# Kernel optimization log

Measured on AMD Instinct MI355X. Metric: run time of the kernel, lower is better.

The kernel has to match this reference:

```python
import jax, jax.numpy as jnp
import numpy as np


def setup_inputs() -> dict:
    key = jax.random.key(0)
    ks = jax.random.split(key, 7)
    B, T, E, H = 4, 4096, 1024, 64
    return {
        "idx": jax.random.normal(ks[0], (B, T, E), dtype=jnp.float32),
        "Wq": jax.random.normal(ks[1], (E, H), dtype=jnp.float32) * (E ** -0.5),
        "bq": jax.random.normal(ks[2], (H,), dtype=jnp.float32) * 0.01,
        "Wk": jax.random.normal(ks[3], (E, H), dtype=jnp.float32) * (E ** -0.5),
        "bk": jax.random.normal(ks[4], (H,), dtype=jnp.float32) * 0.01,
        "Wv": jax.random.normal(ks[5], (E, H), dtype=jnp.float32) * (E ** -0.5),
        "bv": jax.random.normal(ks[6], (H,), dtype=jnp.float32) * 0.01,
    }


def reference(idx, Wq, bq, Wk, bk, Wv, bv):
    # idx: [B, T, E]
    d = idx.shape[-1]  # note: torch code scales by n_embd**-0.5, NOT head_size
    Q = idx @ Wq + bq  # [B, T, H]
    K = idx @ Wk + bk
    V = idx @ Wv + bv
    # scores; NOTE: original torch code calls wei.masked_fill(...) non-in-place
    # and discards the result, so no causal mask is applied. No softmax either.
    wei = jnp.einsum("bth,bsh->bts", Q, K) * (d ** -0.5)  # [B, T, T]
    out = jnp.einsum("bts,bsh->bth", wei, V)  # [B, T, H]
    return out
```

## Files before the change

kernel.cpp:

```cpp
#include <hip/hip_runtime.h>


typedef __attribute__((ext_vector_type(8))) short bf16x8;
typedef __attribute__((ext_vector_type(4))) float f32x4;

#define MFMA16(a, b, c) __builtin_amdgcn_mfma_f32_16x16x32_bf16((a), (b), (c), 0, 0, 0)

__device__ __forceinline__ unsigned short f2bf(float f) {
    unsigned int u = __float_as_uint(f);
    u += 0x7fffu + ((u >> 16) & 1u);
    return (unsigned short)(u >> 16);
}

__global__ void prep(const float* __restrict__ Wq, const float* __restrict__ Wk,
                     const float* __restrict__ Wv, unsigned short* __restrict__ WB,
                     float* __restrict__ Mf) {
    int t = blockIdx.x * 256 + threadIdx.x;
    if (t < 16384) Mf[t] = 0.f;
    int kki = t / 768;
    int rem = t - kki * 768;
    int nt = rem >> 6, lane = rem & 63;
    int n = nt * 16 + (lane & 15);
    int kb = kki * 32 + ((lane >> 4) * 8);
    int mm = n >> 6, h = n & 63;
    const float* W = (mm == 0) ? Wq : (mm == 1) ? Wk : Wv;
    float sc = (mm == 1) ? 0.03125f : 1.0f;
    bf16x8 v;
    #pragma unroll
    for (int j = 0; j < 8; j++) v[j] = (short)f2bf(W[(size_t)(kb + j) * 64 + h] * sc);
    *(bf16x8*)(WB + (size_t)t * 8) = v;
}

__global__ __launch_bounds__(256, 2) void qkv(
    const float* __restrict__ idx, const unsigned short* __restrict__ WB,
    const float* __restrict__ bq, const float* __restrict__ bk, const float* __restrict__ bv,
    unsigned short* __restrict__ Q, unsigned short* __restrict__ Kt,
    unsigned short* __restrict__ Vt) {
    __shared__ unsigned short As[32 * 1032];
    const int lane = threadIdx.x & 63, w = threadIdx.x >> 6;
    const int r0 = blockIdx.x * 32;

    const float* src = idx + (size_t)(r0 + w * 8) * 1024;
    #pragma unroll
    for (int batch = 0; batch < 4; batch++) {
        float4 v[8];
        #pragma unroll
        for (int j = 0; j < 8; j++)
            v[j] = *(const float4*)(src + (size_t)(batch * 8 + j) * 256 + lane * 4);
        #pragma unroll
        for (int j = 0; j < 8; j++) {
            int i   = batch * 8 + j;
            int row = w * 8 + (i >> 2);
            int k   = (i & 3) * 256 + lane * 4;
            unsigned int lo = ((unsigned int)f2bf(v[j].y) << 16) | f2bf(v[j].x);
            unsigned int hi = ((unsigned int)f2bf(v[j].w) << 16) | f2bf(v[j].z);
            uint2 p; p.x = lo; p.y = hi;
            *(uint2*)(As + (size_t)row * 1032 + k) = p;
        }
    }
    __syncthreads();

    const f32x4 z4 = {0.f, 0.f, 0.f, 0.f};
    f32x4 acc[2][3] = {{z4, z4, z4}, {z4, z4, z4}};

    const unsigned short* a_base0 = As + (size_t)(lane & 15) * 1032 + ((lane >> 4) * 8);
    const unsigned short* a_base1 = a_base0 + 16 * 1032;
    bf16x8 a_c[2], b0[3], b1[3], b2[3];
    a_c[0] = *(const bf16x8*)a_base0;
    a_c[1] = *(const bf16x8*)a_base1;
    {
        const unsigned short* Bp0 = WB + (size_t)(lane * 8);
        const unsigned short* Bp1 = WB + (size_t)(12 * 64 + lane) * 8;
        #pragma unroll
        for (int j = 0; j < 3; j++) {
            b0[j] = *(const bf16x8*)(Bp0 + (w + j * 4) * 512);
            b1[j] = *(const bf16x8*)(Bp1 + (w + j * 4) * 512);
            b2[j] = b1[j];
        }
    }
    for (int kk = 0; kk < 32; kk++) {
        bf16x8 na0 = a_c[0], na1 = a_c[1];
        if (kk < 30) {
            const unsigned short* Bp = WB + (size_t)(((kk + 2) * 12) * 64 + lane) * 8;
            #pragma unroll
            for (int j = 0; j < 3; j++) b2[j] = *(const bf16x8*)(Bp + (w + j * 4) * 512);
        }
        if (kk < 31) {
            na0 = *(const bf16x8*)(a_base0 + (kk + 1) * 32);
            na1 = *(const bf16x8*)(a_base1 + (kk + 1) * 32);
        }
        #pragma unroll
        for (int j = 0; j < 3; j++) {
            acc[0][j] = MFMA16(a_c[0], b0[j], acc[0][j]);
            acc[1][j] = MFMA16(a_c[1], b0[j], acc[1][j]);
        }
        #pragma unroll
        for (int j = 0; j < 3; j++) { b0[j] = b1[j]; b1[j] = b2[j]; }
        a_c[0] = na0; a_c[1] = na1;
    }

    __syncthreads();
    unsigned short* Lq = As;
    unsigned short* Lk = As + 2048;
    unsigned short* Lv = As + 4096;
    const int h     = w * 16 + (lane & 15);
    const int rbase = (lane >> 4) * 4;
    {
        float bias0 = bq[h], bias1 = bk[h] * 0.03125f, bias2 = bv[h];
        #pragma unroll
        for (int rf = 0; rf < 2; rf++) {
            #pragma unroll
            for (int reg = 0; reg < 4; reg++) {
                int r = rf * 16 + rbase + reg;
                Lq[r * 64 + h] = f2bf(acc[rf][0][reg] + bias0);
                Lk[h * 32 + r] = f2bf(acc[rf][1][reg] + bias1);
                Lv[h * 32 + r] = f2bf(acc[rf][2][reg] + bias2);
            }
        }
    }
    __syncthreads();
    {
        const int tt = threadIdx.x;
        int qr = tt >> 3, qh = (tt & 7) * 8;
        *(uint4*)(Q + (size_t)(r0 + qr) * 64 + qh) = *(const uint4*)(Lq + qr * 64 + qh);
        int b = r0 >> 12, t0 = r0 & 4095;
        int hh = tt >> 2, tc = (tt & 3) * 8;
        *(uint4*)(Kt + (size_t)b * 262144 + hh * 4096 + t0 + tc) =
            *(const uint4*)(Lk + hh * 32 + tc);
        *(uint4*)(Vt + (size_t)b * 262144 + hh * 4096 + t0 + tc) =
            *(const uint4*)(Lv + hh * 32 + tc);
    }
}

__global__ __launch_bounds__(256) void ktv(
    const unsigned short* __restrict__ Kt, const unsigned short* __restrict__ Vt,
    float* __restrict__ Mf) {
    const int lane = threadIdx.x & 63, wave = threadIdx.x >> 6;
    const int c = blockIdx.x, b = blockIdx.y;
    const unsigned short* Kb = Kt + (size_t)b * 262144;
    const unsigned short* Vb = Vt + (size_t)b * 262144;
    const f32x4 z4 = {0.f, 0.f, 0.f, 0.f};
    f32x4 acc[4] = {z4, z4, z4, z4};
    const int m  = 16 * wave + (lane & 15);
    const int tq = (lane >> 4) * 8;
    #pragma unroll
    for (int it = 0; it < 4; it++) {
        int t0 = c * 128 + it * 32 + tq;
        bf16x8 a = *(const bf16x8*)&Kb[(size_t)m * 4096 + t0];
        #pragma unroll
        for (int nt = 0; nt < 4; nt++) {
            bf16x8 bb = *(const bf16x8*)&Vb[(size_t)(nt * 16 + (lane & 15)) * 4096 + t0];
            acc[nt] = MFMA16(a, bb, acc[nt]);
        }
    }
    float* P = Mf + (size_t)b * 4096;
    const int rowb = 16 * wave + (lane >> 4) * 4;
    #pragma unroll
    for (int nt = 0; nt < 4; nt++)
        #pragma unroll
        for (int reg = 0; reg < 4; reg++)
            atomicAdd(&P[(rowb + reg) * 64 + nt * 16 + (lane & 15)], acc[nt][reg]);
}

__global__ __launch_bounds__(256) void qm(
    const unsigned short* __restrict__ Q, const float* __restrict__ Mf,
    float* __restrict__ out) {
    __shared__ unsigned short Lm[64 * 72];
    const int lane = threadIdx.x & 63, wave = threadIdx.x >> 6;
    const int r0 = blockIdx.x * 64;
    const int b  = r0 >> 12;
    {
        const int tt = threadIdx.x;
        int h1 = tt >> 2, h2c = (tt & 3) * 16;
        const float* Mp = Mf + (size_t)b * 4096 + h1 * 64 + h2c;
        float vals[16];
        *(float4*)(vals + 0)  = *(const float4*)(Mp + 0);
        *(float4*)(vals + 4)  = *(const float4*)(Mp + 4);
        *(float4*)(vals + 8)  = *(const float4*)(Mp + 8);
        *(float4*)(vals + 12) = *(const float4*)(Mp + 12);
        #pragma unroll
        for (int u = 0; u < 16; u++) Lm[(h2c + u) * 72 + h1] = f2bf(vals[u]);
    }
    __syncthreads();
    const f32x4 z4 = {0.f, 0.f, 0.f, 0.f};
    f32x4 acc[4] = {z4, z4, z4, z4};
    const int rr = r0 + 16 * wave + (lane & 15);
    const int kq = (lane >> 4) * 8;
    #pragma unroll
    for (int ks = 0; ks < 2; ks++) {
        int k0 = ks * 32;
        bf16x8 a = *(const bf16x8*)&Q[(size_t)rr * 64 + k0 + kq];
        #pragma unroll
        for (int nt = 0; nt < 4; nt++) {
            bf16x8 bb = *(const bf16x8*)&Lm[(size_t)(nt * 16 + (lane & 15)) * 72 + k0 + kq];
            acc[nt] = MFMA16(a, bb, acc[nt]);
        }
    }
    const int rowb = r0 + 16 * wave + (lane >> 4) * 4;
    #pragma unroll
    for (int nt = 0; nt < 4; nt++)
        #pragma unroll
        for (int reg = 0; reg < 4; reg++)
            out[(size_t)(rowb + reg) * 64 + nt * 16 + (lane & 15)] = acc[nt][reg];
}

extern "C" void kernel_launch(void* const* d_in, const int* in_sizes, int n_in,
                              void* d_out, int out_size, void* d_ws, size_t ws_size,
                              hipStream_t stream) {
    const float* idx = (const float*)d_in[0];
    const float* Wq  = (const float*)d_in[1];
    const float* bq  = (const float*)d_in[2];
    const float* Wk  = (const float*)d_in[3];
    const float* bk  = (const float*)d_in[4];
    const float* Wv  = (const float*)d_in[5];
    const float* bv  = (const float*)d_in[6];
    float* out = (float*)d_out;

    char* ws = (char*)d_ws;
    unsigned short* WB = (unsigned short*)(ws);
    float*          Mf = (float*)(ws + (1024u << 10));
    unsigned short* Q  = (unsigned short*)(ws + (2048u << 10));
    unsigned short* Kt = (unsigned short*)(ws + (4096u << 10));
    unsigned short* Vt = (unsigned short*)(ws + (6144u << 10));

    hipLaunchKernelGGL(prep, dim3(96),    dim3(256), 0, stream, Wq, Wk, Wv, WB, Mf);
    hipLaunchKernelGGL(qkv,  dim3(512),   dim3(256), 0, stream,
                       idx, WB, bq, bk, bv, Q, Kt, Vt);
    hipLaunchKernelGGL(ktv,  dim3(32, 4), dim3(256), 0, stream, Kt, Vt, Mf);
    hipLaunchKernelGGL(qm,   dim3(256),   dim3(256), 0, stream, Q, Mf, out);
}
```

Baseline: 121.9 us.

## Fuse all stages into one cooperative persistent kernel with grid syncs

Replaces the four-kernel pipeline (weight prep, QKV projection, K^T V reduction, Q·M) with a single cooperative kernel that uses grid.sync between phases. Q stays in shared memory across phases, and each block writes a per-block partial K^T V that is then reduced by 64 blocks. This is meant to remove launch gaps and the global round-trip of Q/K/V. The cost is three grid-wide barriers and a larger partial buffer. If the cooperative launch fails, the code falls back to the old kernels.

```diff
diff --git a/kernel.cpp b/kernel.cpp
--- a/kernel.cpp
+++ b/kernel.cpp
@@ -1,4 +1,7 @@
 #include <hip/hip_runtime.h>
+#include <hip/hip_cooperative_groups.h>
+
+namespace cg = cooperative_groups;
 
 
 typedef __attribute__((ext_vector_type(8))) short bf16x8;
@@ -10,6 +13,180 @@
     unsigned int u = __float_as_uint(f);
     u += 0x7fffu + ((u >> 16) & 1u);
     return (unsigned short)(u >> 16);
+}
+
+__global__ __launch_bounds__(256, 2) void mega(
+    const float* __restrict__ idx,
+    const float* __restrict__ Wq, const float* __restrict__ bq_,
+    const float* __restrict__ Wk, const float* __restrict__ bk_,
+    const float* __restrict__ Wv, const float* __restrict__ bv_,
+    unsigned short* __restrict__ WB, float* __restrict__ part,
+    unsigned short* __restrict__ Mt, float* __restrict__ out) {
+    __shared__ unsigned short As[32 * 1032];
+    __shared__ unsigned short Lq[32 * 68];
+    unsigned short* Lk = As;
+    unsigned short* Lv = As + 64 * 36;
+
+    const int tid = threadIdx.x, lane = tid & 63, w = tid >> 6;
+    const int bid = blockIdx.x;
+    cg::grid_group grid = cg::this_grid();
+
+    if (bid < 96) {
+        int t = bid * 256 + tid;
+        int kki = t / 768;
+        int rem = t - kki * 768;
+        int nt = rem >> 6, l = rem & 63;
+        int n = nt * 16 + (l & 15);
+        int kb = kki * 32 + ((l >> 4) * 8);
+        int mm = n >> 6, h = n & 63;
+        const float* W = (mm == 0) ? Wq : (mm == 1) ? Wk : Wv;
+        float sc = (mm == 1) ? 0.03125f : 1.0f;
+        bf16x8 v;
+        #pragma unroll
+        for (int j = 0; j < 8; j++) v[j] = (short)f2bf(W[(size_t)(kb + j) * 64 + h] * sc);
+        *(bf16x8*)(WB + (size_t)t * 8) = v;
+    }
+    grid.sync();
+
+    const int r0 = bid * 32;
+    {
+        const float* src = idx + (size_t)(r0 + w * 8) * 1024;
+        #pragma unroll
+        for (int batch = 0; batch < 4; batch++) {
+            float4 v[8];
+            #pragma unroll
+            for (int j = 0; j < 8; j++)
+                v[j] = *(const float4*)(src + (size_t)(batch * 8 + j) * 256 + lane * 4);
+            #pragma unroll
+            for (int j = 0; j < 8; j++) {
+                int i   = batch * 8 + j;
+                int row = w * 8 + (i >> 2);
+                int k   = (i & 3) * 256 + lane * 4;
+                unsigned int lo = ((unsigned int)f2bf(v[j].y) << 16) | f2bf(v[j].x);
+                unsigned int hi = ((unsigned int)f2bf(v[j].w) << 16) | f2bf(v[j].z);
+                uint2 p; p.x = lo; p.y = hi;
+                *(uint2*)(As + (size_t)row * 1032 + k) = p;
+            }
+        }
+    }
+    __syncthreads();
+
+    const f32x4 z4 = {0.f, 0.f, 0.f, 0.f};
+    f32x4 acc[2][3] = {{z4, z4, z4}, {z4, z4, z4}};
+    {
+        const unsigned short* a_base0 = As + (size_t)(lane & 15) * 1032 + ((lane >> 4) * 8);
+        const unsigned short* a_base1 = a_base0 + 16 * 1032;
+        bf16x8 a_c[2], b0[3], b1[3], b2[3];
+        a_c[0] = *(const bf16x8*)a_base0;
+        a_c[1] = *(const bf16x8*)a_base1;
+        {
+            const unsigned short* Bp0 = WB + (size_t)(lane * 8);
+            const unsigned short* Bp1 = WB + (size_t)(12 * 64 + lane) * 8;
+            #pragma unroll
+            for (int j = 0; j < 3; j++) {
+                b0[j] = *(const bf16x8*)(Bp0 + (w + j * 4) * 512);
+                b1[j] = *(const bf16x8*)(Bp1 + (w + j * 4) * 512);
+                b2[j] = b1[j];
+            }
+        }
+        for (int kk = 0; kk < 32; kk++) {
+            bf16x8 na0 = a_c[0], na1 = a_c[1];
+            if (kk < 30) {
+                const unsigned short* Bp = WB + (size_t)(((kk + 2) * 12) * 64 + lane) * 8;
+                #pragma unroll
+                for (int j = 0; j < 3; j++) b2[j] = *(const bf16x8*)(Bp + (w + j * 4) * 512);
+            }
+            if (kk < 31) {
+                na0 = *(const bf16x8*)(a_base0 + (kk + 1) * 32);
+                na1 = *(const bf16x8*)(a_base1 + (kk + 1) * 32);
+            }
+            #pragma unroll
+            for (int j = 0; j < 3; j++) {
+                acc[0][j] = MFMA16(a_c[0], b0[j], acc[0][j]);
+                acc[1][j] = MFMA16(a_c[1], b0[j], acc[1][j]);
+            }
+            #pragma unroll
+            for (int j = 0; j < 3; j++) { b0[j] = b1[j]; b1[j] = b2[j]; }
+            a_c[0] = na0; a_c[1] = na1;
+        }
+    }
+
+    __syncthreads();
+    {
+        const int h     = w * 16 + (lane & 15);
+        const int rbase = (lane >> 4) * 4;
+        float bias0 = bq_[h], bias1 = bk_[h] * 0.03125f, bias2 = bv_[h];
+        #pragma unroll
+        for (int rf = 0; rf < 2; rf++) {
+            #pragma unroll
+            for (int reg = 0; reg < 4; reg++) {
+                int r = rf * 16 + rbase + reg;
+                Lq[r * 68 + h] = f2bf(acc[rf][0][reg] + bias0);
+                Lk[h * 36 + r] = f2bf(acc[rf][1][reg] + bias1);
+                Lv[h * 36 + r] = f2bf(acc[rf][2][reg] + bias2);
+            }
+        }
+    }
+    __syncthreads();
+
+    {
+        const int tq = (lane >> 4) * 8;
+        bf16x8 a = *(const bf16x8*)&Lk[(16 * w + (lane & 15)) * 36 + tq];
+        f32x4 accM[4];
+        #pragma unroll
+        for (int nt = 0; nt < 4; nt++) {
+            bf16x8 bb = *(const bf16x8*)&Lv[(nt * 16 + (lane & 15)) * 36 + tq];
+            accM[nt] = MFMA16(a, bb, z4);
+        }
+        float* P = part + (size_t)bid * 4096;
+        const int rowb = 16 * w + (lane >> 4) * 4;
+        #pragma unroll
+        for (int nt = 0; nt < 4; nt++)
+            #pragma unroll
+            for (int reg = 0; reg < 4; reg++)
+                P[(rowb + reg) * 64 + nt * 16 + (lane & 15)] = accM[nt][reg];
+    }
+    grid.sync();
+
+    if (bid < 64) {
+        int i = bid * 256 + tid;
+        int b = i >> 12, e = i & 4095;
+        const float* Pp = part + (size_t)(b * 128) * 4096 + e;
+        float s0 = 0.f, s1 = 0.f, s2 = 0.f, s3 = 0.f;
+        #pragma unroll 4
+        for (int j = 0; j < 128; j += 4) {
+            s0 += Pp[(size_t)(j + 0) * 4096];
+            s1 += Pp[(size_t)(j + 1) * 4096];
+            s2 += Pp[(size_t)(j + 2) * 4096];
+            s3 += Pp[(size_t)(j + 3) * 4096];
+        }
+        Mt[(size_t)b * 4096 + (e & 63) * 64 + (e >> 6)] = f2bf((s0 + s1) + (s2 + s3));
+    }
+    grid.sync();
+
+    {
+        const int rf = w >> 1, np = w & 1;
+        const int b  = r0 >> 12;
+        const int kq = (lane >> 4) * 8;
+        f32x4 acc4[2] = {z4, z4};
+        #pragma unroll
+        for (int ks = 0; ks < 2; ks++) {
+            bf16x8 a = *(const bf16x8*)&Lq[(rf * 16 + (lane & 15)) * 68 + ks * 32 + kq];
+            #pragma unroll
+            for (int j = 0; j < 2; j++) {
+                int nt = np * 2 + j;
+                bf16x8 bb = *(const bf16x8*)&Mt[(size_t)b * 4096 +
+                                                (nt * 16 + (lane & 15)) * 64 + ks * 32 + kq];
+                acc4[j] = MFMA16(a, bb, acc4[j]);
+            }
+        }
+        const int rowb = r0 + rf * 16 + (lane >> 4) * 4;
+        #pragma unroll
+        for (int j = 0; j < 2; j++)
+            #pragma unroll
+            for (int reg = 0; reg < 4; reg++)
+                out[(size_t)(rowb + reg) * 64 + (np * 2 + j) * 16 + (lane & 15)] = acc4[j][reg];
+    }
 }
 
 __global__ void prep(const float* __restrict__ Wq, const float* __restrict__ Wk,
@@ -39,7 +216,6 @@
     __shared__ unsigned short As[32 * 1032];
     const int lane = threadIdx.x & 63, w = threadIdx.x >> 6;
     const int r0 = blockIdx.x * 32;
-
     const float* src = idx + (size_t)(r0 + w * 8) * 1024;
     #pragma unroll
     for (int batch = 0; batch < 4; batch++) {
@@ -59,10 +235,8 @@
         }
     }
     __syncthreads();
-
     const f32x4 z4 = {0.f, 0.f, 0.f, 0.f};
     f32x4 acc[2][3] = {{z4, z4, z4}, {z4, z4, z4}};
-
     const unsigned short* a_base0 = As + (size_t)(lane & 15) * 1032 + ((lane >> 4) * 8);
     const unsigned short* a_base1 = a_base0 + 16 * 1032;
     bf16x8 a_c[2], b0[3], b1[3], b2[3];
@@ -98,7 +272,6 @@
         for (int j = 0; j < 3; j++) { b0[j] = b1[j]; b1[j] = b2[j]; }
         a_c[0] = na0; a_c[1] = na1;
     }
-
     __syncthreads();
     unsigned short* Lq = As;
     unsigned short* Lk = As + 2048;
@@ -218,14 +391,23 @@
 
     char* ws = (char*)d_ws;
     unsigned short* WB = (unsigned short*)(ws);
-    float*          Mf = (float*)(ws + (1024u << 10));
-    unsigned short* Q  = (unsigned short*)(ws + (2048u << 10));
-    unsigned short* Kt = (unsigned short*)(ws + (4096u << 10));
-    unsigned short* Vt = (unsigned short*)(ws + (6144u << 10));
-
-    hipLaunchKernelGGL(prep, dim3(96),    dim3(256), 0, stream, Wq, Wk, Wv, WB, Mf);
-    hipLaunchKernelGGL(qkv,  dim3(512),   dim3(256), 0, stream,
-                       idx, WB, bq, bk, bv, Q, Kt, Vt);
-    hipLaunchKernelGGL(ktv,  dim3(32, 4), dim3(256), 0, stream, Kt, Vt, Mf);
-    hipLaunchKernelGGL(qm,   dim3(256),   dim3(256), 0, stream, Q, Mf, out);
-}
+    float*          Pp = (float*)(ws + (1024u << 10));
+    unsigned short* Mt = (unsigned short*)(ws + (9216u << 10));
+
+    void* args[] = {(void*)&idx, (void*)&Wq, (void*)&bq, (void*)&Wk, (void*)&bk,
+                    (void*)&Wv, (void*)&bv, (void*)&WB, (void*)&Pp, (void*)&Mt,
+                    (void*)&out};
+    hipError_t e = hipLaunchCooperativeKernel((const void*)mega, dim3(512), dim3(256),
+                                              args, 0, stream);
+    if (e != hipSuccess) {
+        float*          Mf = (float*)(ws + (16384u << 10));
+        unsigned short* Q  = (unsigned short*)(ws + (17408u << 10));
+        unsigned short* Kt = (unsigned short*)(ws + (19456u << 10));
+        unsigned short* Vt = (unsigned short*)(ws + (21504u << 10));
+        hipLaunchKernelGGL(prep, dim3(96),    dim3(256), 0, stream, Wq, Wk, Wv, WB, Mf);
+        hipLaunchKernelGGL(qkv,  dim3(512),   dim3(256), 0, stream,
+                           idx, WB, bq, bk, bv, Q, Kt, Vt);
+        hipLaunchKernelGGL(ktv,  dim3(32, 4), dim3(256), 0, stream, Kt, Vt, Mf);
+        hipLaunchKernelGGL(qm,   dim3(256),   dim3(256), 0, stream, Q, Mf, out);
+    }
+}
```

Measured after the change: 302.9 us. 148% more time.

## Fuse K^T V partial product into QKV projection kernel, drop Kt/Vt round trip

Applied to the files above, without the earlier changes.

The separate ktv kernel is removed. Each qkv block now computes its own 32-row K^T V contribution from the K and V tiles held in shared memory and atomically adds it into Mf. This avoids writing Kt/Vt to global memory, reading them back, and one kernel launch. The cost is many more atomics: 512 blocks each add a 64x64 partial instead of 128 blocks. Shared-memory padding was also changed (strides 68 and 36) to reduce bank conflicts.

```diff
diff --git a/kernel.cpp b/kernel.cpp
--- a/kernel.cpp
+++ b/kernel.cpp
@@ -31,135 +31,120 @@
     *(bf16x8*)(WB + (size_t)t * 8) = v;
 }
 
-__global__ __launch_bounds__(256, 2) void qkv(
+__global__ __launch_bounds__(256, 2) void qkv_m(
     const float* __restrict__ idx, const unsigned short* __restrict__ WB,
     const float* __restrict__ bq, const float* __restrict__ bk, const float* __restrict__ bv,
-    unsigned short* __restrict__ Q, unsigned short* __restrict__ Kt,
-    unsigned short* __restrict__ Vt) {
+    unsigned short* __restrict__ Q, float* __restrict__ Mf) {
     __shared__ unsigned short As[32 * 1032];
-    const int lane = threadIdx.x & 63, w = threadIdx.x >> 6;
+    __shared__ unsigned short Lq[32 * 68];
+    unsigned short* Lk = As;
+    unsigned short* Lv = As + 64 * 36;
+
+    const int tid = threadIdx.x, lane = tid & 63, w = tid >> 6;
     const int r0 = blockIdx.x * 32;
 
-    const float* src = idx + (size_t)(r0 + w * 8) * 1024;
-    #pragma unroll
-    for (int batch = 0; batch < 4; batch++) {
-        float4 v[8];
-        #pragma unroll
-        for (int j = 0; j < 8; j++)
-            v[j] = *(const float4*)(src + (size_t)(batch * 8 + j) * 256 + lane * 4);
-        #pragma unroll
-        for (int j = 0; j < 8; j++) {
-            int i   = batch * 8 + j;
-            int row = w * 8 + (i >> 2);
-            int k   = (i & 3) * 256 + lane * 4;
-            unsigned int lo = ((unsigned int)f2bf(v[j].y) << 16) | f2bf(v[j].x);
-            unsigned int hi = ((unsigned int)f2bf(v[j].w) << 16) | f2bf(v[j].z);
-            uint2 p; p.x = lo; p.y = hi;
-            *(uint2*)(As + (size_t)row * 1032 + k) = p;
+    {
+        const float* src = idx + (size_t)(r0 + w * 8) * 1024;
+        #pragma unroll
+        for (int batch = 0; batch < 4; batch++) {
+            float4 v[8];
+            #pragma unroll
+            for (int j = 0; j < 8; j++)
+                v[j] = *(const float4*)(src + (size_t)(batch * 8 + j) * 256 + lane * 4);
+            #pragma unroll
+            for (int j = 0; j < 8; j++) {
+                int i   = batch * 8 + j;
+                int row = w * 8 + (i >> 2);
+                int k   = (i & 3) * 256 + lane * 4;
+                unsigned int lo = ((unsigned int)f2bf(v[j].y) << 16) | f2bf(v[j].x);
+                unsigned int hi = ((unsigned int)f2bf(v[j].w) << 16) | f2bf(v[j].z);
+                uint2 p; p.x = lo; p.y = hi;
+                *(uint2*)(As + (size_t)row * 1032 + k) = p;
+            }
         }
     }
     __syncthreads();
 
     const f32x4 z4 = {0.f, 0.f, 0.f, 0.f};
     f32x4 acc[2][3] = {{z4, z4, z4}, {z4, z4, z4}};
-
-    const unsigned short* a_base0 = As + (size_t)(lane & 15) * 1032 + ((lane >> 4) * 8);
-    const unsigned short* a_base1 = a_base0 + 16 * 1032;
-    bf16x8 a_c[2], b0[3], b1[3], b2[3];
-    a_c[0] = *(const bf16x8*)a_base0;
-    a_c[1] = *(const bf16x8*)a_base1;
-    {
-        const unsigned short* Bp0 = WB + (size_t)(lane * 8);
-        const unsigned short* Bp1 = WB + (size_t)(12 * 64 + lane) * 8;
-        #pragma unroll
-        for (int j = 0; j < 3; j++) {
-            b0[j] = *(const bf16x8*)(Bp0 + (w + j * 4) * 512);
-            b1[j] = *(const bf16x8*)(Bp1 + (w + j * 4) * 512);
-            b2[j] = b1[j];
-        }
-    }
-    for (int kk = 0; kk < 32; kk++) {
-        bf16x8 na0 = a_c[0], na1 = a_c[1];
-        if (kk < 30) {
-            const unsigned short* Bp = WB + (size_t)(((kk + 2) * 12) * 64 + lane) * 8;
-            #pragma unroll
-            for (int j = 0; j < 3; j++) b2[j] = *(const bf16x8*)(Bp + (w + j * 4) * 512);
-        }
-        if (kk < 31) {
-            na0 = *(const bf16x8*)(a_base0 + (kk + 1) * 32);
-            na1 = *(const bf16x8*)(a_base1 + (kk + 1) * 32);
-        }
-        #pragma unroll
-        for (int j = 0; j < 3; j++) {
-            acc[0][j] = MFMA16(a_c[0], b0[j], acc[0][j]);
-            acc[1][j] = MFMA16(a_c[1], b0[j], acc[1][j]);
-        }
-        #pragma unroll
-        for (int j = 0; j < 3; j++) { b0[j] = b1[j]; b1[j] = b2[j]; }
-        a_c[0] = na0; a_c[1] = na1;
-    }
-
-    __syncthreads();
-    unsigned short* Lq = As;
-    unsigned short* Lk = As + 2048;
-    unsigned short* Lv = As + 4096;
-    const int h     = w * 16 + (lane & 15);
-    const int rbase = (lane >> 4) * 4;
-    {
+    {
+        const unsigned short* a_base0 = As + (size_t)(lane & 15) * 1032 + ((lane >> 4) * 8);
+        const unsigned short* a_base1 = a_base0 + 16 * 1032;
+        bf16x8 a_c[2], b0[3], b1[3], b2[3];
+        a_c[0] = *(const bf16x8*)a_base0;
+        a_c[1] = *(const bf16x8*)a_base1;
+        {
+            const unsigned short* Bp0 = WB + (size_t)(lane * 8);
+            const unsigned short* Bp1 = WB + (size_t)(12 * 64 + lane) * 8;
+            #pragma unroll
+            for (int j = 0; j < 3; j++) {
+                b0[j] = *(const bf16x8*)(Bp0 + (w + j * 4) * 512);
+                b1[j] = *(const bf16x8*)(Bp1 + (w + j * 4) * 512);
+                b2[j] = b1[j];
+            }
+        }
+        for (int kk = 0; kk < 32; kk++) {
+            bf16x8 na0 = a_c[0], na1 = a_c[1];
+            if (kk < 30) {
+                const unsigned short* Bp = WB + (size_t)(((kk + 2) * 12) * 64 + lane) * 8;
+                #pragma unroll
+                for (int j = 0; j < 3; j++) b2[j] = *(const bf16x8*)(Bp + (w + j * 4) * 512);
+            }
+            if (kk < 31) {
+                na0 = *(const bf16x8*)(a_base0 + (kk + 1) * 32);
+                na1 = *(const bf16x8*)(a_base1 + (kk + 1) * 32);
+            }
+            #pragma unroll
+            for (int j = 0; j < 3; j++) {
+                acc[0][j] = MFMA16(a_c[0], b0[j], acc[0][j]);
+                acc[1][j] = MFMA16(a_c[1], b0[j], acc[1][j]);
+            }
+            #pragma unroll
+            for (int j = 0; j < 3; j++) { b0[j] = b1[j]; b1[j] = b2[j]; }
+            a_c[0] = na0; a_c[1] = na1;
+        }
+    }
+
+    __syncthreads();
+    {
+        const int h     = w * 16 + (lane & 15);
+        const int rbase = (lane >> 4) * 4;
         float bias0 = bq[h], bias1 = bk[h] * 0.03125f, bias2 = bv[h];
         #pragma unroll
         for (int rf = 0; rf < 2; rf++) {
             #pragma unroll
             for (int reg = 0; reg < 4; reg++) {
                 int r = rf * 16 + rbase + reg;
-                Lq[r * 64 + h] = f2bf(acc[rf][0][reg] + bias0);
-                Lk[h * 32 + r] = f2bf(acc[rf][1][reg] + bias1);
-                Lv[h * 32 + r] = f2bf(acc[rf][2][reg] + bias2);
-            }
-        }
-    }
-    __syncthreads();
-    {
-        const int tt = threadIdx.x;
-        int qr = tt >> 3, qh = (tt & 7) * 8;
-        *(uint4*)(Q + (size_t)(r0 + qr) * 64 + qh) = *(const uint4*)(Lq + qr * 64 + qh);
-        int b = r0 >> 12, t0 = r0 & 4095;
-        int hh = tt >> 2, tc = (tt & 3) * 8;
-        *(uint4*)(Kt + (size_t)b * 262144 + hh * 4096 + t0 + tc) =
-            *(const uint4*)(Lk + hh * 32 + tc);
-        *(uint4*)(Vt + (size_t)b * 262144 + hh * 4096 + t0 + tc) =
-            *(const uint4*)(Lv + hh * 32 + tc);
-    }
-}
-
-__global__ __launch_bounds__(256) void ktv(
-    const unsigned short* __restrict__ Kt, const unsigned short* __restrict__ Vt,
-    float* __restrict__ Mf) {
-    const int lane = threadIdx.x & 63, wave = threadIdx.x >> 6;
-    const int c = blockIdx.x, b = blockIdx.y;
-    const unsigned short* Kb = Kt + (size_t)b * 262144;
-    const unsigned short* Vb = Vt + (size_t)b * 262144;
-    const f32x4 z4 = {0.f, 0.f, 0.f, 0.f};
-    f32x4 acc[4] = {z4, z4, z4, z4};
-    const int m  = 16 * wave + (lane & 15);
-    const int tq = (lane >> 4) * 8;
-    #pragma unroll
-    for (int it = 0; it < 4; it++) {
-        int t0 = c * 128 + it * 32 + tq;
-        bf16x8 a = *(const bf16x8*)&Kb[(size_t)m * 4096 + t0];
+                Lq[r * 68 + h] = f2bf(acc[rf][0][reg] + bias0);
+                Lk[h * 36 + r] = f2bf(acc[rf][1][reg] + bias1);
+                Lv[h * 36 + r] = f2bf(acc[rf][2][reg] + bias2);
+            }
+        }
+    }
+    __syncthreads();
+
+    {
+        int qr = tid >> 3, qh = (tid & 7) * 8;
+        *(uint4*)(Q + (size_t)(r0 + qr) * 64 + qh) = *(const uint4*)(Lq + qr * 68 + qh);
+    }
+
+    {
+        const int tq = (lane >> 4) * 8;
+        bf16x8 a = *(const bf16x8*)&Lk[(16 * w + (lane & 15)) * 36 + tq];
+        f32x4 accM[4];
         #pragma unroll
         for (int nt = 0; nt < 4; nt++) {
-            bf16x8 bb = *(const bf16x8*)&Vb[(size_t)(nt * 16 + (lane & 15)) * 4096 + t0];
-            acc[nt] = MFMA16(a, bb, acc[nt]);
-        }
-    }
-    float* P = Mf + (size_t)b * 4096;
-    const int rowb = 16 * wave + (lane >> 4) * 4;
-    #pragma unroll
-    for (int nt = 0; nt < 4; nt++)
-        #pragma unroll
-        for (int reg = 0; reg < 4; reg++)
-            atomicAdd(&P[(rowb + reg) * 64 + nt * 16 + (lane & 15)], acc[nt][reg]);
+            bf16x8 bb = *(const bf16x8*)&Lv[(nt * 16 + (lane & 15)) * 36 + tq];
+            accM[nt] = MFMA16(a, bb, z4);
+        }
+        float* P = Mf + (size_t)(r0 >> 12) * 4096;
+        const int rowb = 16 * w + (lane >> 4) * 4;
+        #pragma unroll
+        for (int nt = 0; nt < 4; nt++)
+            #pragma unroll
+            for (int reg = 0; reg < 4; reg++)
+                atomicAdd(&P[(rowb + reg) * 64 + nt * 16 + (lane & 15)], accM[nt][reg]);
+    }
 }
 
 __global__ __launch_bounds__(256) void qm(
@@ -220,12 +205,9 @@
     unsigned short* WB = (unsigned short*)(ws);
     float*          Mf = (float*)(ws + (1024u << 10));
     unsigned short* Q  = (unsigned short*)(ws + (2048u << 10));
-    unsigned short* Kt = (unsigned short*)(ws + (4096u << 10));
-    unsigned short* Vt = (unsigned short*)(ws + (6144u << 10));
-
-    hipLaunchKernelGGL(prep, dim3(96),    dim3(256), 0, stream, Wq, Wk, Wv, WB, Mf);
-    hipLaunchKernelGGL(qkv,  dim3(512),   dim3(256), 0, stream,
-                       idx, WB, bq, bk, bv, Q, Kt, Vt);
-    hipLaunchKernelGGL(ktv,  dim3(32, 4), dim3(256), 0, stream, Kt, Vt, Mf);
-    hipLaunchKernelGGL(qm,   dim3(256),   dim3(256), 0, stream, Q, Mf, out);
-}
+
+    hipLaunchKernelGGL(prep,  dim3(96),  dim3(256), 0, stream, Wq, Wk, Wv, WB, Mf);
+    hipLaunchKernelGGL(qkv_m, dim3(512), dim3(256), 0, stream,
+                       idx, WB, bq, bk, bv, Q, Mf);
+    hipLaunchKernelGGL(qm,    dim3(256), dim3(256), 0, stream, Q, Mf, out);
+}
```

Result: no change. 123.5 us (+1.2%).
